# Kernel tuning notes

Hardware: AMD Instinct MI355X
Metric: run time of the kernel (lower is better)

## Reference

```python
import jax, jax.numpy as jnp
import numpy as np
import math

MAX_L = 8                       # spherical-harmonic max degree
R = 0.95                        # poincare disk radius
ENERGY_THR = 0.9999
GOLDEN = 0.618033988749
LM = [(l, m) for l in range(MAX_L + 1) for m in range(-l, l + 1)]  # 81 pairs


def _assoc_legendre(x, l, m):
    # m >= 0, standard upward recurrence; x is a vector
    if l == 0 and m == 0:
        return jnp.ones_like(x)
    pmm = jnp.ones_like(x)
    if m > 0:
        somx2 = jnp.sqrt(1.0 - x * x)
        fact = 1.0
        for _ in range(m):
            pmm = pmm * (-fact * somx2)
            fact += 2.0
    if l == m:
        return pmm
    pmmp1 = x * (2 * m + 1) * pmm
    if l == m + 1:
        return pmmp1
    pll, plp1 = pmm, pmmp1
    for ll in range(m + 2, l + 1):
        pnew = ((2 * ll - 1) * x * plp1 - (ll + m - 1) * pll) / (ll - m)
        pll, plp1 = plp1, pnew
    return plp1


def _harmonic(cos_t, phi, l, m):
    P = _assoc_legendre(cos_t, l, abs(m))
    norm = math.sqrt((2 * l + 1) * math.factorial(l - abs(m))
                     / math.factorial(l + abs(m)) / (4.0 * math.pi))
    ang = jnp.cos(m * phi) if m >= 0 else jnp.sin(abs(m) * phi)
    return norm * P * ang


def _sphere_coords(zr, zi):
    # hyperbolic radius -> polar angle on sphere; phi = complex argument
    r = jnp.sqrt(zr * zr + zi * zi)
    phi = jnp.arctan2(zi, zr)
    cos_t = jnp.cos(2.0 * jnp.arctanh(jnp.minimum(r, 0.99)) * math.pi / (2.0 * MAX_L))
    return cos_t, phi


def _forward_transform(w):
    flat = w.reshape(-1)
    if flat.shape[0] % 2 == 1:
        flat = jnp.concatenate([flat, jnp.zeros((1,), flat.dtype)])
    re, im = flat[0::2], flat[1::2]
    mag = jnp.sqrt(re * re + im * im)
    scale = jnp.max(mag)
    safe = jnp.where(scale > 0, scale, 1.0)
    a, b = re / safe, im / safe
    # complex tanh(a+ib) = (sinh 2a + i sin 2b) / (cosh 2a + cos 2b)
    den = jnp.cosh(2 * a) + jnp.cos(2 * b)
    pr = jnp.where(scale > 0, jnp.sinh(2 * a) / den * R, re)
    pi_ = jnp.where(scale > 0, jnp.sin(2 * b) / den * R, im)
    cos_t, phi = _sphere_coords(pr, pi_)
    coeffs = jnp.stack([jnp.mean(_harmonic(cos_t, phi, l, m)) for l, m in LM])
    return coeffs, scale, re.shape[0]


def _compress(c):
    # adaptive top-energy masking (decompress restores zeros -> masking is exact)
    n = c.shape[0]
    mag = jnp.abs(c)
    order = jnp.argsort(-mag)
    e = jnp.cumsum(mag[order] ** 2)
    tot = e[-1]
    kc = jnp.where(tot > 0,
                   jnp.sum(e / jnp.maximum(tot, 1e-30) <= ENERGY_THR) + 1,
                   n)
    kc = jnp.maximum(kc, n // 2)
    ranks = jnp.zeros((n,), jnp.int32).at[order].set(jnp.arange(n, dtype=jnp.int32))
    return jnp.where(ranks < kc, c, 0.0)


def _inverse_transform(c, scale, num_points, shape):
    i = jnp.arange(num_points, dtype=jnp.float32)
    r = jnp.minimum((i + 0.5) / num_points * R, 0.95)
    theta = jnp.mod(2.0 * math.pi * i * GOLDEN, 1.0)
    zr, zi = r * jnp.cos(theta), r * jnp.sin(theta)
    cos_t, phi = _sphere_coords(zr, zi)
    cm = jnp.where(jnp.abs(c) > 1e-10, c, 0.0)
    recon = jnp.zeros((num_points,), jnp.float32)
    for idx, (l, m) in enumerate(LM):
        recon = recon + cm[idx] * _harmonic(cos_t, phi, l, m)
    real = jnp.where(scale > 0, recon * scale, recon)
    # interleave (real, imag=0) as in torch stack([re, im], 1).flatten()
    flat = jnp.stack([real, jnp.zeros_like(real)], axis=1).reshape(-1)
    total = int(np.prod(shape))
    if flat.shape[0] > total:
        flat = flat[:total]
    elif flat.shape[0] < total:
        flat = jnp.concatenate([flat, jnp.zeros((total - flat.shape[0],), flat.dtype)])
    return flat.reshape(shape)


def setup_inputs() -> dict:
    key = jax.random.key(0)
    ks = jax.random.split(key, 5)
    return {
        "x": jax.random.normal(ks[0], (8, 1024, 768), jnp.float32),
        "w_fc": jax.random.normal(ks[1], (2, 3072, 768), jnp.float32) * 0.02,
        "w_proj": jax.random.normal(ks[2], (2, 768, 3072), jnp.float32) * 0.02,
        "b_fc": jax.random.normal(ks[3], (2, 3072), jnp.float32) * 0.02,
        "b_proj": jax.random.normal(ks[4], (2, 768), jnp.float32) * 0.02,
    }


def reference(x, w_fc, w_proj, b_fc, b_proj):
    L = w_fc.shape[0]
    imp = jax.nn.softmax(jnp.arange(L, dtype=jnp.float32) * 0.5)
    fused_fc = jnp.einsum('l,lij->ij', imp, w_fc)
    fused_proj = jnp.einsum('l,lij->ij', imp, w_proj)
    bias_fc = jnp.einsum('l,li->i', imp, b_fc)
    bias_proj = jnp.einsum('l,li->i', imp, b_proj)

    c_fc, s_fc, n_fc = _forward_transform(fused_fc)
    W_fc = _inverse_transform(_compress(c_fc), s_fc, n_fc, fused_fc.shape)
    c_pr, s_pr, n_pr = _forward_transform(fused_proj)
    W_proj = _inverse_transform(_compress(c_pr), s_pr, n_pr, fused_proj.shape)

    h = jax.nn.gelu(jnp.einsum('bsd,fd->bsf', x, W_fc) + bias_fc, approximate=False)
    return jnp.einsum('bsf,df->bsd', h, W_proj) + bias_proj
```

## Files before the change

kernel.cpp:

```cpp
#include <hip/hip_runtime.h>

#define MAXL 8
#define NC 81
#define NPAIR 1179648
#define TOTW  2359296
#define PI_F 3.14159265358979323846f
#define CO_BLOCKS 256

typedef __attribute__((ext_vector_type(8))) __bf16 bf16x8;
typedef __attribute__((ext_vector_type(4))) float f32x4;
typedef __attribute__((address_space(3))) void lds_void;
typedef const __attribute__((address_space(1))) void glb_void;

constexpr double cfact(int n){ double r=1.0; for(int i=2;i<=n;++i) r*=(double)i; return r; }
constexpr double csqrtd(double x){
  double r = (x > 1.0) ? x : 1.0;
  for (int i=0;i<200;++i) r = 0.5*(r + x/r);
  return r;
}
struct Norms { float v[NC]; };
constexpr Norms make_norms(){
  Norms t{};
  for (int l=0;l<=MAXL;++l)
    for (int m=-l;m<=l;++m){
      int am = m<0?-m:m;
      double nn = csqrtd((double)(2*l+1)*cfact(l-am)/cfact(l+am)/(4.0*3.14159265358979323846));
      t.v[l*l+l+m] = (float)nn;
    }
  return t;
}
__constant__ Norms g_norm = make_norms();

__device__ __forceinline__ float fast_atanh(float x){
  return 0.5f * __logf((1.0f + x) * __builtin_amdgcn_rcpf(1.0f - x));
}

__global__ __launch_bounds__(256) void k_max(const float* __restrict__ wfc,
    const float* __restrict__ wpr, int* __restrict__ scaleBits,
    double* __restrict__ gacc, float imp0, float imp1){
  const int mat = blockIdx.y;
  if (mat == 0 && blockIdx.x == 0 && threadIdx.x < 2*NC) gacc[threadIdx.x] = 0.0;
  const float2* w0 = (const float2*)(mat ? wpr : wfc);
  const float2* w1 = w0 + (TOTW/2);
  float vmax = 0.0f;
  for (int i = blockIdx.x*blockDim.x + threadIdx.x; i < NPAIR; i += gridDim.x*blockDim.x){
    float2 a = w0[i], b = w1[i];
    float re = fmaf(imp0, a.x, imp1*b.x);
    float im = fmaf(imp0, a.y, imp1*b.y);
    vmax = fmaxf(vmax, sqrtf(re*re + im*im));
  }
  for (int off=32; off; off>>=1) vmax = fmaxf(vmax, __shfl_down(vmax, off));
  __shared__ float red[4];
  int lane = threadIdx.x & 63, wv = threadIdx.x >> 6;
  if (lane == 0) red[wv] = vmax;
  __syncthreads();
  if (threadIdx.x == 0){
    float m = fmaxf(fmaxf(red[0], red[1]), fmaxf(red[2], red[3]));
    atomicMax(scaleBits + mat, (int)__float_as_uint(m));
  }
}

__global__ __launch_bounds__(256,2) void k_coeff(const float* __restrict__ wfc,
                                                 const float* __restrict__ wpr,
                                                 const unsigned* __restrict__ scaleBits,
                                                 double* __restrict__ gacc,
                                                 const float* __restrict__ x,
                                                 __bf16* __restrict__ A1){
  const int mat = blockIdx.y;

  {
    const int g0 = (mat*CO_BLOCKS + blockIdx.x)*256 + threadIdx.x;
    const int gs = 2*CO_BLOCKS*256;
    #pragma unroll 4
    for (int t = g0; t < 8192*384; t += gs){
      float2 v = ((const float2*)x)[t];
      A1[t] = (__bf16)v.x;
    }
  }

  const float2* w0 = (const float2*)(mat ? wpr : wfc);
  const float2* w1 = w0 + (TOTW/2);
  const float scale = __uint_as_float(scaleBits[mat]);
  const bool has = scale > 0.0f;
  const float inv_safe = 1.0f / (has ? scale : 1.0f);
  const float imp0 = (float)0.37754066879814546;
  const float imp1 = (float)0.62245933120185454;

  float acc[NC];
  #pragma unroll
  for (int v=0; v<NC; ++v) acc[v] = 0.0f;

  auto map1 = [&](int idx, float& X, float& c1, float& s1, float& st){
    float2 av = w0[idx], bv = w1[idx];
    float re = fmaf(imp0, av.x, imp1*bv.x);
    float im = fmaf(imp0, av.y, imp1*bv.y);
    float pr, pi_;
    if (has){
      float a = re*inv_safe, b = im*inv_safe;
      float e  = __expf(2.0f*a);
      float ie = __builtin_amdgcn_rcpf(e);
      float ch = 0.5f*(e + ie), sh = 0.5f*(e - ie);
      float s2b, c2b; __sincosf(2.0f*b, &s2b, &c2b);
      float inv_den = __builtin_amdgcn_rcpf(ch + c2b);
      pr  = sh*inv_den*0.95f;
      pi_ = s2b*inv_den*0.95f;
    } else { pr = re; pi_ = im; }
    float r2 = pr*pr + pi_*pi_;
    float inv_r = (r2 > 0.0f) ? __builtin_amdgcn_rsqf(r2) : 0.0f;
    c1 = (r2 > 0.0f) ? pr*inv_r : 1.0f;
    s1 = pi_*inv_r;
    float rr_ = r2*inv_r;
    float arg = fast_atanh(fminf(rr_, 0.99f)) * (PI_F/8.0f);
    __sincosf(arg, &st, &X);
  };

  const int T = CO_BLOCKS*256;
  for (int i = blockIdx.x*blockDim.x + threadIdx.x; i < NPAIR/2; i += T){
    float X0,c10,s10,st0, X1,c11,s11,st1;
    map1(i,           X0, c10, s10, st0);
    map1(i + NPAIR/2, X1, c11, s11, st1);

    float cm0=1.0f, sm0=0.0f, pm0=1.0f;
    float cm1=1.0f, sm1=0.0f, pm1=1.0f;
    float fact=1.0f;
    #pragma unroll
    for (int m=0; m<=MAXL; ++m){
      if (m > 0){
        float t0 = cm0*c10 - sm0*s10; sm0 = sm0*c10 + cm0*s10; cm0 = t0;
        float t1 = cm1*c11 - sm1*s11; sm1 = sm1*c11 + cm1*s11; cm1 = t1;
        pm0 = pm0 * (-fact*st0);
        pm1 = pm1 * (-fact*st1);
        fact += 2.0f;
      }
      float a1 = pm0, b1 = pm1;
      acc[m*m + 2*m] += a1*cm0 + b1*cm1;
      if (m > 0) acc[m*m] += a1*sm0 + b1*sm1;
      if (m < MAXL){
        float a0 = a1, b0 = b1;
        a1 = X0*(float)(2*m+1)*a0;
        b1 = X1*(float)(2*m+1)*b0;
        acc[(m+1)*(m+1) + (m+1) + m] += a1*cm0 + b1*cm1;
        if (m > 0) acc[(m+1)*(m+1) + 1] += a1*sm0 + b1*sm1;
        #pragma unroll
        for (int l=m+2; l<=MAXL; ++l){
          float an = ((float)(2*l-1)*X0*a1 - (float)(l+m-1)*a0) * (1.0f/(float)(l-m));
          a0 = a1; a1 = an;
          float bn = ((float)(2*l-1)*X1*b1 - (float)(l+m-1)*b0) * (1.0f/(float)(l-m));
          b0 = b1; b1 = bn;
          acc[l*l + l + m] += a1*cm0 + b1*cm1;
          if (m > 0) acc[l*l + l - m] += a1*sm0 + b1*sm1;
        }
      }
    }
  }

  __shared__ float redf[4][NC];
  int lane = threadIdx.x & 63, wv = threadIdx.x >> 6;
  #pragma unroll
  for (int v=0; v<NC; ++v){
    float d = acc[v];
    for (int off=32; off; off>>=1) d += __shfl_down(d, off);
    if (lane == 0) redf[wv][v] = d;
  }
  __syncthreads();
  for (int v = threadIdx.x; v < NC; v += blockDim.x){
    double s = (double)redf[0][v] + (double)redf[1][v] + (double)redf[2][v] + (double)redf[3][v];
    unsafeAtomicAdd(gacc + mat*NC + v, s);
  }
}

__global__ __launch_bounds__(128) void k_compress(const double* __restrict__ gacc,
                                                  float* __restrict__ cfin){
  const int mat = blockIdx.x;
  const int v = threadIdx.x;
  __shared__ float mg[NC];
  __shared__ float smg2[NC];
  __shared__ int cnt_sh;

  float c = 0.0f, m = -1.0f;
  if (v < NC){
    double m_ = (double)g_norm.v[v] * gacc[mat*NC + v] / (double)NPAIR;
    c = (float)m_;
    m = fabsf(c);
    mg[v] = m;
  }
  if (v == 0) cnt_sh = 0;
  __syncthreads();

  int rank = 0;
  if (v < NC){
    #pragma unroll 1
    for (int u = 0; u < NC; ++u){
      float mu = mg[u];
      rank += (mu > m) || (mu == m && u < v);
    }
    smg2[rank] = m*m;
  }
  __syncthreads();

  float e_mine = 0.0f, tot = 0.0f;
  if (v < NC){
    float run = 0.0f;
    #pragma unroll 1
    for (int u = 0; u < NC; ++u){
      run += smg2[u];
      if (u == rank) e_mine = run;
    }
    tot = run;
    float den = fmaxf(tot, 1e-30f);
    if (tot > 0.0f && (e_mine / den <= 0.9999f)) atomicAdd(&cnt_sh, 1);
  }
  __syncthreads();

  if (v < NC){
    int kc = (tot > 0.0f) ? (cnt_sh + 1) : NC;
    if (kc < NC/2) kc = NC/2;
    float cv = (rank < kc) ? c : 0.0f;
    if (fabsf(cv) <= 1e-10f) cv = 0.0f;
    cfin[mat*NC + v] = cv;
  }
}

__global__ __launch_bounds__(256) void k_inverse(const float* __restrict__ cfin,
    const unsigned* __restrict__ scaleBits, __bf16* __restrict__ B1, __bf16* __restrict__ B2){
  __shared__ float cA[NC], cB[NC], sc[2];
  if (threadIdx.x < NC){ cA[threadIdx.x] = cfin[threadIdx.x]; cB[threadIdx.x] = cfin[NC + threadIdx.x]; }
  if (threadIdx.x < 2) sc[threadIdx.x] = __uint_as_float(scaleBits[threadIdx.x]);
  __syncthreads();
  int j = blockIdx.x*blockDim.x + threadIdx.x;
  if (j >= NPAIR) return;

  float jf = (float)j;
  float r = fminf((jf + 0.5f) / 1179648.0f * 0.95f, 0.95f);
  float theta = fmodf((6.28318530717958647692f * jf) * 0.618033988749f, 1.0f);
  float phi = theta;
  float X, sint;
  {
    float arg = fast_atanh(fminf(r, 0.99f)) * (PI_F/8.0f);
    __sincosf(arg, &sint, &X);
  }
  float s1, c1; __sincosf(phi, &s1, &c1);

  float ra = 0.0f, rb = 0.0f;
  float cm = 1.0f, sm = 0.0f, pmm = 1.0f, fact = 1.0f;

  auto emit = [&](int l, int m, float P){
    int ip = l*l + l + m;
    float y = g_norm.v[ip] * P;
    float yc = y*cm;
    ra += cA[ip]*yc; rb += cB[ip]*yc;
    if (m > 0){
      int in_ = l*l + l - m;
      float ys = y*sm;
      ra += cA[in_]*ys; rb += cB[in_]*ys;
    }
  };

  #pragma unroll
  for (int m=0; m<=MAXL; ++m){
    if (m > 0){
      float t = cm*c1 - sm*s1;
      sm = sm*c1 + cm*s1;
      cm = t;
      pmm = pmm * (-fact*sint);
      fact += 2.0f;
    }
    float p0 = pmm;
    emit(m, m, p0);
    if (m < MAXL){
      float p1 = X*(float)(2*m+1)*p0;
      emit(m+1, m, p1);
      #pragma unroll
      for (int l=m+2; l<=MAXL; ++l){
        float pn = ((float)(2*l-1)*X*p1 - (float)(l+m-1)*p0) * (1.0f/(float)(l-m));
        p0 = p1; p1 = pn;
        emit(l, m, p1);
      }
    }
  }

  float sA = sc[0], sB = sc[1];
  B2[j] = (__bf16)((sB > 0.0f) ? rb*sB : rb);
  int q = j / 768, rem = j - q*768;
  if (rem < 384)
    B1[q*384 + rem] = (__bf16)((sA > 0.0f) ? ra*sA : ra);
}

template<int ACT, int OUTBF, int MI, int NJ>
__global__ __launch_bounds__(256) void k_gemm_mfma(
    const __bf16* __restrict__ A, const __bf16* __restrict__ B,
    const float* __restrict__ bias, int bmul, int blen,
    float imp0, float imp1,
    __bf16* __restrict__ Hout, float* __restrict__ Fout,
    int N, int K)
{
  constexpr int BM = 2*MI*16, BN = 2*NJ*16;
  constexpr int ACH = BM/16, NCH = (BM+BN)/16;
  static_assert(NCH % 4 == 0, "chunks must split across 4 waves");
  __shared__ __bf16 As[2][BM*32];
  __shared__ __bf16 Bs[2][BN*32];
  const int tid  = threadIdx.x;
  const int wave = tid >> 6, lane = tid & 63;
  const int wr = wave >> 1, wc = wave & 1;
  const int rr = lane & 15, kq = lane >> 4;
  const int sx = rr & 3;
  const int bm = blockIdx.y * BM, bn = blockIdx.x * BN;

  const int lrow  = lane >> 2;
  const int lslot = lane & 3;
  const int sslot = lslot ^ (lrow & 3);
  const __bf16* Abase = A + (size_t)bm * K;
  const __bf16* Bbase = B + (size_t)bn * K;

  f32x4 acc[MI][NJ] = {};

  auto stage = [&](int buf, int k0){
    #pragma unroll
    for (int is = 0; is < NCH/4; ++is) {
      const int c = is * 4 + wave;
      if (c < ACH) {
        const __bf16* ga = Abase + (size_t)(c*16 + lrow) * K + (k0 + sslot*8);
        __builtin_amdgcn_global_load_lds((glb_void*)ga, (lds_void*)(&As[buf][c*512]), 16, 0, 0);
      } else {
        const int cb = c - ACH;
        const __bf16* gb = Bbase + (size_t)(cb*16 + lrow) * K + (k0 + sslot*8);
        __builtin_amdgcn_global_load_lds((glb_void*)gb, (lds_void*)(&Bs[buf][cb*512]), 16, 0, 0);
      }
    }
  };

  const int nt = K/32;
  stage(0, 0);
  __syncthreads();

  for (int t = 0; t < nt; ++t) {
    const int cur = t & 1;
    if (t + 1 < nt) stage(cur ^ 1, (t+1)*32);

    bf16x8 af[MI], bfr[NJ];
    #pragma unroll
    for (int i=0;i<MI;++i){
      const int row = wr*MI*16 + i*16 + rr;
      af[i]  = *(const bf16x8*)&As[cur][row*32 + ((kq ^ sx) << 3)];
    }
    #pragma unroll
    for (int j=0;j<NJ;++j){
      const int row = wc*NJ*16 + j*16 + rr;
      bfr[j] = *(const bf16x8*)&Bs[cur][row*32 + ((kq ^ sx) << 3)];
    }
    #pragma unroll
    for (int i=0;i<MI;++i)
      #pragma unroll
      for (int j=0;j<NJ;++j)
        acc[i][j] = __builtin_amdgcn_mfma_f32_16x16x32_bf16(af[i], bfr[j], acc[i][j], 0, 0, 0);

    __syncthreads();
  }

  #pragma unroll
  for (int j=0;j<NJ;++j){
    const int col = bn + wc*NJ*16 + j*16 + rr;
    const float bb = imp0*bias[bmul*col] + imp1*bias[blen + bmul*col];
    #pragma unroll
    for (int i=0;i<MI;++i){
      const int row0 = bm + wr*MI*16 + i*16 + kq*4;
      #pragma unroll
      for (int t=0;t<4;++t){
        float v = acc[i][j][t] + bb;
        if (ACT) v = 0.5f*v*(1.0f + erff(v*0.70710678118654752440f));
        if (OUTBF) Hout[(size_t)(row0+t)*N + col] = (__bf16)v;
        else       Fout[(size_t)(row0+t)*N + col] = v;
      }
    }
  }
}

extern "C" void kernel_launch(void* const* d_in, const int* in_sizes, int n_in,
                              void* d_out, int out_size, void* d_ws, size_t ws_size,
                              hipStream_t stream){
  const float* x   = (const float*)d_in[0];
  const float* wfc = (const float*)d_in[1];
  const float* wpr = (const float*)d_in[2];
  const float* bfc = (const float*)d_in[3];
  const float* bpr = (const float*)d_in[4];
  float* out = (float*)d_out;

  char* ws = (char*)d_ws;
  size_t off = 0;
  auto alloc = [&](size_t bytes){ void* p = ws + off; off = (off + bytes + 255) & ~(size_t)255; return p; };

  unsigned* scaleBits= (unsigned*)alloc(8);
  double* gacc       = (double*)  alloc(2*NC*sizeof(double));
  float* cfin        = (float*)   alloc(2*NC*sizeof(float));
  __bf16* B1         = (__bf16*)  alloc((size_t)1536*384*sizeof(__bf16));
  __bf16* B2         = (__bf16*)  alloc((size_t)768*1536*sizeof(__bf16));
  __bf16* A1         = (__bf16*)  alloc((size_t)8192*384*sizeof(__bf16));
  __bf16* H          = (__bf16*)  alloc((size_t)8192*1536*sizeof(__bf16));

  const float imp0 = (float)0.37754066879814546;
  const float imp1 = (float)0.62245933120185454;

  k_max<<<dim3(256,2),256,0,stream>>>(wfc, wpr, (int*)scaleBits, gacc, imp0, imp1);
  k_coeff<<<dim3(CO_BLOCKS,2),256,0,stream>>>(wfc, wpr, scaleBits, gacc, x, A1);
  k_compress<<<2,128,0,stream>>>(gacc, cfin);
  k_inverse<<<4608,256,0,stream>>>(cfin, scaleBits, B1, B2);
  k_gemm_mfma<1,1,4,4><<<dim3(12,64),256,0,stream>>>(A1, B1, bfc, 2, 3072, imp0, imp1, H, nullptr, 1536, 384);
  k_gemm_mfma<0,0,4,4><<<dim3(6,64),256,0,stream>>>(H, B2, bpr, 1, 768, imp0, imp1, nullptr, out, 768, 1536);
}
```

Measured before the change: 165.2 us.

## Split harmonic coefficient accumulation across waves by m-range via LDS-staged points

The coefficient kernel now maps each chunk of 512 points into shared memory, then each of the four waves accumulates only a subset of m orders (0-1, 2-3, 4-5, 6-8) over all staged points. Each thread holds at most 26 accumulators instead of 81, which cuts register pressure, and each wave flushes its own range with double atomics. The grid grows from 256 to 576 blocks per matrix, with fixed 4-chunk coverage. In exchange it adds barriers and LDS traffic, and the wave workloads are uneven (the 6-8 wave does less recurrence work but covers three orders), so the waves can be imbalanced.

```diff
diff --git a/kernel.cpp b/kernel.cpp
--- a/kernel.cpp
+++ b/kernel.cpp
@@ -5,7 +5,9 @@
 #define NPAIR 1179648
 #define TOTW  2359296
 #define PI_F 3.14159265358979323846f
-#define CO_BLOCKS 256
+#define CO_BLOCKS 576
+#define CHUNK 512
+#define NCHUNKS 4
 
 typedef __attribute__((ext_vector_type(8))) __bf16 bf16x8;
 typedef __attribute__((ext_vector_type(4))) float f32x4;
@@ -60,6 +62,56 @@
   }
 }
 
+template<int ML, int MH, int N>
+__device__ __forceinline__ void accum_pt(float X, float c1, float s1, float st, float (&acc)[N]){
+  float cm=1.0f, sm=0.0f, pmm=1.0f, fact=1.0f;
+  #pragma unroll
+  for (int m=1; m<=ML; ++m){
+    float t = cm*c1 - sm*s1; sm = sm*c1 + cm*s1; cm = t;
+    pmm = pmm * (-fact*st); fact += 2.0f;
+  }
+  int k = 0;
+  #pragma unroll
+  for (int m=ML; m<=MH; ++m){
+    if (m > ML){
+      float t = cm*c1 - sm*s1; sm = sm*c1 + cm*s1; cm = t;
+      pmm = pmm * (-fact*st); fact += 2.0f;
+    }
+    float p1 = pmm, p0 = pmm;
+    acc[k++] += p1*cm;
+    if (m > 0) acc[k++] += p1*sm;
+    #pragma unroll
+    for (int l=m+1; l<=MAXL; ++l){
+      float pn;
+      if (l == m+1) pn = X*(float)(2*m+1)*p1;
+      else          pn = ((float)(2*l-1)*X*p1 - (float)(l+m-1)*p0) * (1.0f/(float)(l-m));
+      p0 = p1; p1 = pn;
+      acc[k++] += p1*cm;
+      if (m > 0) acc[k++] += p1*sm;
+    }
+  }
+}
+
+template<int ML, int MH, int N>
+__device__ __forceinline__ void flush_range(float (&acc)[N], int lane, double* __restrict__ gout){
+  int k = 0;
+  #pragma unroll
+  for (int m=ML; m<=MH; ++m)
+    #pragma unroll
+    for (int l=m; l<=MAXL; ++l){
+      {
+        float d = acc[k++];
+        for (int o=32; o; o>>=1) d += __shfl_down(d, o);
+        if (lane == 0) unsafeAtomicAdd(gout + (l*l + l + m), (double)d);
+      }
+      if (m > 0){
+        float d = acc[k++];
+        for (int o=32; o; o>>=1) d += __shfl_down(d, o);
+        if (lane == 0) unsafeAtomicAdd(gout + (l*l + l - m), (double)d);
+      }
+    }
+}
+
 __global__ __launch_bounds__(256,2) void k_coeff(const float* __restrict__ wfc,
                                                  const float* __restrict__ wpr,
                                                  const unsigned* __restrict__ scaleBits,
@@ -71,12 +123,13 @@
   {
     const int g0 = (mat*CO_BLOCKS + blockIdx.x)*256 + threadIdx.x;
     const int gs = 2*CO_BLOCKS*256;
-    #pragma unroll 4
     for (int t = g0; t < 8192*384; t += gs){
       float2 v = ((const float2*)x)[t];
       A1[t] = (__bf16)v.x;
     }
   }
+
+  __shared__ float sX[CHUNK], sC[CHUNK], sS[CHUNK], sT[CHUNK];
 
   const float2* w0 = (const float2*)(mat ? wpr : wfc);
   const float2* w1 = w0 + (TOTW/2);
@@ -85,10 +138,7 @@
   const float inv_safe = 1.0f / (has ? scale : 1.0f);
   const float imp0 = (float)0.37754066879814546;
   const float imp1 = (float)0.62245933120185454;
-
-  float acc[NC];
-  #pragma unroll
-  for (int v=0; v<NC; ++v) acc[v] = 0.0f;
+  const int wv = threadIdx.x >> 6, lane = threadIdx.x & 63;
 
   auto map1 = [&](int idx, float& X, float& c1, float& s1, float& st){
     float2 av = w0[idx], bv = w1[idx];
@@ -114,59 +164,41 @@
     __sincosf(arg, &st, &X);
   };
 
-  const int T = CO_BLOCKS*256;
-  for (int i = blockIdx.x*blockDim.x + threadIdx.x; i < NPAIR/2; i += T){
-    float X0,c10,s10,st0, X1,c11,s11,st1;
-    map1(i,           X0, c10, s10, st0);
-    map1(i + NPAIR/2, X1, c11, s11, st1);
-
-    float cm0=1.0f, sm0=0.0f, pm0=1.0f;
-    float cm1=1.0f, sm1=0.0f, pm1=1.0f;
-    float fact=1.0f;
-    #pragma unroll
-    for (int m=0; m<=MAXL; ++m){
-      if (m > 0){
-        float t0 = cm0*c10 - sm0*s10; sm0 = sm0*c10 + cm0*s10; cm0 = t0;
-        float t1 = cm1*c11 - sm1*s11; sm1 = sm1*c11 + cm1*s11; cm1 = t1;
-        pm0 = pm0 * (-fact*st0);
-        pm1 = pm1 * (-fact*st1);
-        fact += 2.0f;
-      }
-      float a1 = pm0, b1 = pm1;
-      acc[m*m + 2*m] += a1*cm0 + b1*cm1;
-      if (m > 0) acc[m*m] += a1*sm0 + b1*sm1;
-      if (m < MAXL){
-        float a0 = a1, b0 = b1;
-        a1 = X0*(float)(2*m+1)*a0;
-        b1 = X1*(float)(2*m+1)*b0;
-        acc[(m+1)*(m+1) + (m+1) + m] += a1*cm0 + b1*cm1;
-        if (m > 0) acc[(m+1)*(m+1) + 1] += a1*sm0 + b1*sm1;
-        #pragma unroll
-        for (int l=m+2; l<=MAXL; ++l){
-          float an = ((float)(2*l-1)*X0*a1 - (float)(l+m-1)*a0) * (1.0f/(float)(l-m));
-          a0 = a1; a1 = an;
-          float bn = ((float)(2*l-1)*X1*b1 - (float)(l+m-1)*b0) * (1.0f/(float)(l-m));
-          b0 = b1; b1 = bn;
-          acc[l*l + l + m] += a1*cm0 + b1*cm1;
-          if (m > 0) acc[l*l + l - m] += a1*sm0 + b1*sm1;
-        }
-      }
-    }
-  }
-
-  __shared__ float redf[4][NC];
-  int lane = threadIdx.x & 63, wv = threadIdx.x >> 6;
-  #pragma unroll
-  for (int v=0; v<NC; ++v){
-    float d = acc[v];
-    for (int off=32; off; off>>=1) d += __shfl_down(d, off);
-    if (lane == 0) redf[wv][v] = d;
-  }
-  __syncthreads();
-  for (int v = threadIdx.x; v < NC; v += blockDim.x){
-    double s = (double)redf[0][v] + (double)redf[1][v] + (double)redf[2][v] + (double)redf[3][v];
-    unsafeAtomicAdd(gacc + mat*NC + v, s);
-  }
+  float acc[26];
+  #pragma unroll
+  for (int v=0; v<26; ++v) acc[v] = 0.0f;
+
+  for (int c = 0; c < NCHUNKS; ++c){
+    {
+      const int pb = (c*CO_BLOCKS + blockIdx.x)*CHUNK;
+      float X0,C0,S0,T0, X1,C1,S1,T1;
+      map1(pb + threadIdx.x,        X0, C0, S0, T0);
+      map1(pb + threadIdx.x + 256,  X1, C1, S1, T1);
+      sX[threadIdx.x]     = X0; sC[threadIdx.x]     = C0; sS[threadIdx.x]     = S0; sT[threadIdx.x]     = T0;
+      sX[threadIdx.x+256] = X1; sC[threadIdx.x+256] = C1; sS[threadIdx.x+256] = S1; sT[threadIdx.x+256] = T1;
+    }
+    __syncthreads();
+    if (wv == 0){
+      #pragma unroll 2
+      for (int j=0;j<8;++j){ int s = 64*j + lane; accum_pt<0,1>(sX[s], sC[s], sS[s], sT[s], acc); }
+    } else if (wv == 1){
+      #pragma unroll 2
+      for (int j=0;j<8;++j){ int s = 64*j + lane; accum_pt<2,3>(sX[s], sC[s], sS[s], sT[s], acc); }
+    } else if (wv == 2){
+      #pragma unroll 2
+      for (int j=0;j<8;++j){ int s = 64*j + lane; accum_pt<4,5>(sX[s], sC[s], sS[s], sT[s], acc); }
+    } else {
+      #pragma unroll 2
+      for (int j=0;j<8;++j){ int s = 64*j + lane; accum_pt<6,8>(sX[s], sC[s], sS[s], sT[s], acc); }
+    }
+    __syncthreads();
+  }
+
+  double* gout = gacc + mat*NC;
+  if      (wv == 0) flush_range<0,1>(acc, lane, gout);
+  else if (wv == 1) flush_range<2,3>(acc, lane, gout);
+  else if (wv == 2) flush_range<4,5>(acc, lane, gout);
+  else              flush_range<6,8>(acc, lane, gout);
 }
 
 __global__ __launch_bounds__(128) void k_compress(const double* __restrict__ gacc,
```

Result: slower. 274.9 us (+66.5%).
